# Kernel optimization log

Hardware: AMD Instinct MI355X
Metric: run time of the kernel (lower is better)

## Reference

```python
import jax, jax.numpy as jnp
import numpy as np

EPS = 1e-5

def setup_inputs() -> dict:
    key = jax.random.key(0)
    ks = jax.random.split(key, 8)
    B, C, O, H, W = 4, 256, 256, 64, 64
    x = jax.random.normal(ks[0], (B, C, H, W), jnp.float32)
    # offset/mask conv: 27 = deformable_groups(1) * 3 * kh * kw; small init so sampling points stay near grid
    w_off = jax.random.normal(ks[1], (27, C, 3, 3), jnp.float32) * 0.01
    b_off = jnp.zeros((27,), jnp.float32)
    weight = jax.random.normal(ks[2], (O, C, 3, 3), jnp.float32) * (1.0 / np.sqrt(C * 9))
    bias = jnp.zeros((O,), jnp.float32)
    gamma = 1.0 + 0.1 * jax.random.normal(ks[3], (O,), jnp.float32)
    beta = 0.1 * jax.random.normal(ks[4], (O,), jnp.float32)
    run_mean = 0.05 * jax.random.normal(ks[5], (O,), jnp.float32)
    run_var = jax.random.uniform(ks[6], (O,), jnp.float32, 0.5, 1.5)
    return {"x": x, "w_off": w_off, "b_off": b_off, "weight": weight, "bias": bias,
            "gamma": gamma, "beta": beta, "run_mean": run_mean, "run_var": run_var}

def reference(x, w_off, b_off, weight, bias, gamma, beta, run_mean, run_var):
    B, C, H, W = x.shape
    O = weight.shape[0]
    K = 9  # 3x3 kernel taps
    # conv_offset_mask: standard 3x3 conv, pad 1 -> (B, 27, H, W)
    om = jax.lax.conv_general_dilated(
        x, w_off, window_strides=(1, 1), padding=[(1, 1), (1, 1)],
        dimension_numbers=("NCHW", "OIHW", "NCHW")) + b_off[None, :, None, None]
    dy, dx = om[:, :K], om[:, K:2 * K]            # (B,9,H,W) learned offsets
    mask = jax.nn.sigmoid(om[:, 2 * K:])           # (B,9,H,W) modulation
    # base sampling grid for 3x3, stride 1, pad 1, dilation 1
    ky, kx = jnp.meshgrid(jnp.arange(3), jnp.arange(3), indexing="ij")
    ky = ky.reshape(K, 1, 1).astype(x.dtype)
    kx = kx.reshape(K, 1, 1).astype(x.dtype)
    base_y = (jnp.arange(H, dtype=x.dtype) - 1.0)[None, :, None] + ky  # (9,H,1)
    base_x = (jnp.arange(W, dtype=x.dtype) - 1.0)[None, None, :] + kx  # (9,1,W)
    py = dy + base_y  # (B,9,H,W) absolute sample coords
    px = dx + base_x
    y0 = jnp.floor(py); x0 = jnp.floor(px)
    ly = py - y0; lx = px - x0
    y0i = y0.astype(jnp.int32); x0i = x0.astype(jnp.int32)
    xf = x.reshape(B, C, H * W)

    def corner(yi, xi, wgt):
        valid = (yi >= 0) & (yi < H) & (xi >= 0) & (xi < W)  # zero-pad outside
        yc = jnp.clip(yi, 0, H - 1)
        xc = jnp.clip(xi, 0, W - 1)
        idx = (yc * W + xc).reshape(B, 1, -1)                # (B,1,9HW)
        g = jnp.take_along_axis(xf, idx, axis=2)             # (B,C,9HW)
        return g * (wgt * valid.astype(x.dtype)).reshape(B, 1, -1)

    val = (corner(y0i, x0i, (1 - ly) * (1 - lx))
           + corner(y0i, x0i + 1, (1 - ly) * lx)
           + corner(y0i + 1, x0i, ly * (1 - lx))
           + corner(y0i + 1, x0i + 1, ly * lx))
    val = val.reshape(B, C, K, H, W) * mask[:, None]          # modulated im2col
    out = jnp.einsum("bckhw,ock->bohw", val, weight.reshape(O, C, K))
    out = out + bias[None, :, None, None]
    # BN (eval mode, running stats) + ReLU
    inv = jax.lax.rsqrt(run_var + EPS)
    out = gamma[None, :, None, None] * (out - run_mean[None, :, None, None]) * inv[None, :, None, None] + beta[None, :, None, None]
    return jax.nn.relu(out)
```

## Files before the change

kernel.cpp:

```cpp
#include <hip/hip_runtime.h>
#include <math.h>

#define HW_ 4096
#define N_ 16384
#define RS 592

typedef _Float16 f16x4 __attribute__((ext_vector_type(4)));
typedef _Float16 f16x8 __attribute__((ext_vector_type(8)));
typedef float f32x4 __attribute__((ext_vector_type(4)));


static __device__ __forceinline__ unsigned short f2h(float f) {
  _Float16 h = (_Float16)f;
  return __builtin_bit_cast(unsigned short, h);
}
static __device__ __forceinline__ f32x4 madv(f32x4 a, float s, f32x4 c) {
  c.x = fmaf(a.x, s, c.x);
  c.y = fmaf(a.y, s, c.y);
  c.z = fmaf(a.z, s, c.z);
  c.w = fmaf(a.w, s, c.w);
  return c;
}

__global__ __launch_bounds__(256) void setup_kernel(
    const float* __restrict__ x, const float* __restrict__ weight,
    const float* __restrict__ w_off, const float* __restrict__ bias,
    const float* __restrict__ gamma, const float* __restrict__ beta,
    const float* __restrict__ rmean, const float* __restrict__ rvar,
    unsigned short* __restrict__ Wt, unsigned short* __restrict__ Woff,
    float* __restrict__ scale, float* __restrict__ shift, float* __restrict__ xT) {
  int bid = blockIdx.x;
  int tid = threadIdx.x;
  if (bid < 1024) {
    __shared__ float t[64][65];
    int b = bid >> 8, cg = (bid >> 6) & 3, h = bid & 63;
    int wl = tid & 63, c4 = tid >> 6;
#pragma unroll
    for (int j = 0; j < 16; ++j) {
      int cl = j * 4 + c4;
      t[cl][wl] = x[(size_t)(b * 256 + cg * 64 + cl) * HW_ + h * 64 + wl];
    }
    __syncthreads();
    int cl2 = tid & 63, w4g = tid >> 6;
#pragma unroll
    for (int j = 0; j < 16; ++j) {
      int w2 = j * 4 + w4g;
      xT[(size_t)(b * HW_ + h * 64 + w2) * 256 + cg * 64 + cl2] = t[cl2][w2];
    }
    return;
  }
  int o = bid - 1024;
#pragma unroll
  for (int j = 0; j < 9; ++j) {
    int wk = tid + j * 256;
    int cb = wk / 288;
    int rem = wk - cb * 288;
    int k = rem >> 5, cloc = rem & 31;
    int c = cb * 32 + cloc;
    Wt[((cb * 9 + k) * 256 + o) * 32 + cloc] = f2h(weight[(size_t)(o * 256 + c) * 9 + k]);
    if (o < 32) {
      float wv = (o < 27) ? w_off[(size_t)(o * 256 + c) * 9 + k] : 0.f;
      Woff[((cb * 9 + k) * 32 + o) * 32 + cloc] = f2h(wv);
    }
  }
  if (o == 0) {
    float inv = rsqrtf(rvar[tid] + 1e-5f);
    float sc = gamma[tid] * inv;
    scale[tid] = sc;
    shift[tid] = beta[tid] + sc * (bias[tid] - rmean[tid]);
  }
}

__global__ __launch_bounds__(512) void fused_kernel(
    const float* __restrict__ xT, const unsigned short* __restrict__ Wt,
    const unsigned short* __restrict__ Woff, const float* __restrict__ b_off,
    const float* __restrict__ scale, const float* __restrict__ shift,
    float* __restrict__ out) {
  __shared__ __align__(16) char smem[64 * RS];
  float* om_lds = (float*)smem;
  unsigned int* pk_lds = (unsigned int*)(smem + 8192);
  float* w4_lds = (float*)(smem + 10496);

  int bid = blockIdx.x;
  int swz = (bid & 7) * 32 + (bid >> 3);
  int nbase = swz * 64;
  int b = nbase >> 12;
  int h = (nbase >> 6) & 63;

  int tid = threadIdx.x;
  int lane = tid & 63;
  int wv = tid >> 6;
  int m15 = lane & 15, q = lane >> 4;
  int sn = tid >> 3;
  int cs = tid & 7;

  const char* xb = (const char*)xT + (size_t)b * (HW_ * 256 * 4);

  int mf = wv >> 2, nf1 = wv & 3;
  f32x4 aoff = (f32x4){0.f, 0.f, 0.f, 0.f};
  for (int cb = 0; cb < 8; ++cb) {
    {
      const char* xc = xb + (size_t)(cb * 32 + cs * 4) * 4;
      char* ldr = smem + sn * RS + cs * 8;
#pragma unroll
      for (int k = 0; k < 9; ++k) {
        int ky = k / 3, kx = k - 3 * (k / 3);
        int yy = h + ky - 1, xx = sn + kx - 1;
        f32x4 v = (f32x4){0.f, 0.f, 0.f, 0.f};
        if (((unsigned)yy < 64u) && ((unsigned)xx < 64u))
          v = *(const f32x4*)(xc + (size_t)(yy * 64 + xx) * 1024);
        *(f16x4*)(ldr + k * 64) = __builtin_convertvector(v, f16x4);
      }
    }
    __syncthreads();
#pragma unroll
    for (int ks = 0; ks < 9; ++ks) {
      f16x8 a = *(const f16x8*)(Woff + ((cb * 9 + ks) * 32 + mf * 16 + m15) * 32 + q * 8);
      f16x8 bb = *(const f16x8*)(smem + (nf1 * 16 + m15) * RS + ks * 64 + q * 16);
      aoff = __builtin_amdgcn_mfma_f32_16x16x32_f16(a, bb, aoff, 0, 0, 0);
    }
    __syncthreads();
  }
#pragma unroll
  for (int r = 0; r < 4; ++r)
    om_lds[(mf * 16 + q * 4 + r) * 64 + nf1 * 16 + m15] = aoff[r];
  __syncthreads();

  for (int it = tid; it < 576; it += 512) {
    int k = it >> 6, px = it & 63;
    float dy = om_lds[k * 64 + px] + b_off[k];
    float dx = om_lds[(k + 9) * 64 + px] + b_off[k + 9];
    float z = om_lds[(k + 18) * 64 + px] + b_off[k + 18];
    float ms = 1.f / (1.f + expf(-z));
    int ky = k / 3, kx = k - 3 * ky;
    float py = dy + (float)(h - 1 + ky);
    float pxf = dx + (float)(px - 1 + kx);
    float fy0 = floorf(py), fx0 = floorf(pxf);
    float ly = py - fy0, lx = pxf - fx0;
    int iy0 = (int)fy0, ix0 = (int)fx0;
    bool vy0 = (iy0 >= 0) && (iy0 < 64);
    bool vy1 = (iy0 >= -1) && (iy0 < 63);
    bool vx0 = (ix0 >= 0) && (ix0 < 64);
    bool vx1 = (ix0 >= -1) && (ix0 < 63);
    int yA = min(max(iy0, 0), 63), yB = min(max(iy0 + 1, 0), 63);
    int xA = min(max(ix0, 0), 63), xB = min(max(ix0 + 1, 0), 63);
    pk_lds[k * 64 + px] = (unsigned)(yA * 64 + xA) | ((unsigned)(xB - xA) << 12) |
                          ((unsigned)(yB - yA) << 13);
    float* wp = w4_lds + (k * 64 + px) * 4;
    wp[0] = (1.f - ly) * (1.f - lx) * ms * ((vy0 && vx0) ? 1.f : 0.f);
    wp[1] = (1.f - ly) * lx * ms * ((vy0 && vx1) ? 1.f : 0.f);
    wp[2] = ly * (1.f - lx) * ms * ((vy1 && vx0) ? 1.f : 0.f);
    wp[3] = ly * lx * ms * ((vy1 && vx1) ? 1.f : 0.f);
  }
  __syncthreads();

  unsigned int pkv[9];
  float wf[9][4];
#pragma unroll
  for (int k = 0; k < 9; ++k) {
    pkv[k] = pk_lds[k * 64 + sn];
#pragma unroll
    for (int j = 0; j < 4; ++j) wf[k][j] = w4_lds[(k * 64 + sn) * 4 + j];
  }

  f32x4 acc[2][4];
#pragma unroll
  for (int mfi = 0; mfi < 2; ++mfi)
#pragma unroll
    for (int nf = 0; nf < 4; ++nf) acc[mfi][nf] = (f32x4){0.f, 0.f, 0.f, 0.f};

  f16x4 sv[9];
#define GATHER(CB)                                                     \
  {                                                                    \
    const char* xc = xb + (CB) * 128 + cs * 16;                        \
    _Pragma("unroll") for (int k = 0; k < 9; ++k) {                    \
      unsigned pv = pkv[k];                                            \
      const char* p00 = xc + ((size_t)(pv & 0xFFFu) << 10);            \
      int dxb = (int)(pv & 0x1000u) >> 2;             \
      int dyb = (int)(pv & 0x2000u) << 3;             \
      f32x4 c00 = *(const f32x4*)(p00);                                \
      f32x4 c01 = *(const f32x4*)(p00 + dxb);                          \
      f32x4 c10 = *(const f32x4*)(p00 + dyb);                          \
      f32x4 c11 = *(const f32x4*)(p00 + dyb + dxb);                    \
      f32x4 v = (f32x4){0.f, 0.f, 0.f, 0.f};                           \
      v = madv(c00, wf[k][0], v);                                      \
      v = madv(c01, wf[k][1], v);                                      \
      v = madv(c10, wf[k][2], v);                                      \
      v = madv(c11, wf[k][3], v);                                      \
      sv[k] = __builtin_convertvector(v, f16x4);                       \
    }                                                                  \
  }

  GATHER(0);
  __syncthreads();
  for (int cb = 0; cb < 8; ++cb) {
    {
      char* ldr = smem + sn * RS + cs * 8;
#pragma unroll
      for (int k = 0; k < 9; ++k) *(f16x4*)(ldr + k * 64) = sv[k];
    }
    __syncthreads();
    if (cb < 7) GATHER(cb + 1);
    {
      const unsigned short* wtk = Wt + (size_t)(cb * 9) * 8192 + (wv * 32 + m15) * 32 + q * 8;
#pragma unroll
      for (int ks = 0; ks < 9; ++ks) {
        const unsigned short* wp2 = wtk + ks * 8192;
        f16x8 a0 = *(const f16x8*)(wp2);
        f16x8 a1 = *(const f16x8*)(wp2 + 512);
#pragma unroll
        for (int nf = 0; nf < 4; ++nf) {
          f16x8 bb = *(const f16x8*)(smem + (nf * 16 + m15) * RS + ks * 64 + q * 16);
          acc[0][nf] = __builtin_amdgcn_mfma_f32_16x16x32_f16(a0, bb, acc[0][nf], 0, 0, 0);
          acc[1][nf] = __builtin_amdgcn_mfma_f32_16x16x32_f16(a1, bb, acc[1][nf], 0, 0, 0);
        }
      }
    }
    __syncthreads();
  }

  float* ob = out + (size_t)(b * 256) * HW_ + h * 64;
#pragma unroll
  for (int mfi = 0; mfi < 2; ++mfi)
#pragma unroll
    for (int r = 0; r < 4; ++r) {
      int o = wv * 32 + mfi * 16 + q * 4 + r;
      float sc = scale[o], sh = shift[o];
#pragma unroll
      for (int nf = 0; nf < 4; ++nf) {
        float vv = fmaxf(fmaf(acc[mfi][nf][r], sc, sh), 0.f);
        ob[(size_t)o * HW_ + nf * 16 + m15] = vv;
      }
    }
}

extern "C" void kernel_launch(void* const* d_in, const int* in_sizes, int n_in,
                              void* d_out, int out_size, void* d_ws, size_t ws_size,
                              hipStream_t stream) {
  (void)in_sizes; (void)n_in; (void)out_size; (void)ws_size;
  const float* x = (const float*)d_in[0];
  const float* w_off = (const float*)d_in[1];
  const float* b_off = (const float*)d_in[2];
  const float* weight = (const float*)d_in[3];
  const float* bias = (const float*)d_in[4];
  const float* gamma = (const float*)d_in[5];
  const float* beta = (const float*)d_in[6];
  const float* rmean = (const float*)d_in[7];
  const float* rvar = (const float*)d_in[8];
  char* ws = (char*)d_ws;
  unsigned short* Wt = (unsigned short*)ws;
  unsigned short* Woff = (unsigned short*)(ws + 1179648);
  float* scale = (float*)(ws + 1327104);
  float* shift = (float*)(ws + 1328128);
  float* xT = (float*)(ws + 1329152);
  float* out = (float*)d_out;

  setup_kernel<<<dim3(1280), dim3(256), 0, stream>>>(x, weight, w_off, bias, gamma, beta,
                                                     rmean, rvar, Wt, Woff, scale, shift, xT);
  fused_kernel<<<dim3(256), dim3(512), 0, stream>>>(xT, Wt, Woff, b_off, scale, shift, out);
}
```

Baseline: 192.2 us.

## Halve pixel tile per block, double channel chunk, vectorize transpose setup

The fused deformable-conv kernel now processes 32 output pixels per block instead of 64. It launches 512 blocks so more of the GPU's compute units are busy, and channels are staged in chunks of 64 with a reordered weight layout (18 k-steps per chunk). The setup transpose now uses float4 loads and stores with fewer, larger blocks. Smaller tiles double the weight reads from global/L2 per output, and the offset conv uses only half the waves.

Result: slower. 245.3 us (+27.6%).

```diff
diff --git a/kernel.cpp b/kernel.cpp
--- a/kernel.cpp
+++ b/kernel.cpp
@@ -3,7 +3,7 @@
 
 #define HW_ 4096
 #define N_ 16384
-#define RS 592
+#define RS2 1168
 
 typedef _Float16 f16x4 __attribute__((ext_vector_type(4)));
 typedef _Float16 f16x8 __attribute__((ext_vector_type(8)));
@@ -22,7 +22,7 @@
   return c;
 }
 
-__global__ __launch_bounds__(256) void setup_kernel(
+__global__ __launch_bounds__(512) void setup_kernel(
     const float* __restrict__ x, const float* __restrict__ weight,
     const float* __restrict__ w_off, const float* __restrict__ bias,
     const float* __restrict__ gamma, const float* __restrict__ beta,
@@ -31,110 +31,125 @@
     float* __restrict__ scale, float* __restrict__ shift, float* __restrict__ xT) {
   int bid = blockIdx.x;
   int tid = threadIdx.x;
-  if (bid < 1024) {
+  if (bid < 256) {
     __shared__ float t[64][65];
-    int b = bid >> 8, cg = (bid >> 6) & 3, h = bid & 63;
-    int wl = tid & 63, c4 = tid >> 6;
-#pragma unroll
-    for (int j = 0; j < 16; ++j) {
-      int cl = j * 4 + c4;
-      t[cl][wl] = x[(size_t)(b * 256 + cg * 64 + cl) * HW_ + h * 64 + wl];
-    }
-    __syncthreads();
-    int cl2 = tid & 63, w4g = tid >> 6;
-#pragma unroll
-    for (int j = 0; j < 16; ++j) {
-      int w2 = j * 4 + w4g;
-      xT[(size_t)(b * HW_ + h * 64 + w2) * 256 + cg * 64 + cl2] = t[cl2][w2];
+    int b = bid >> 6, h = bid & 63;
+    int cq = tid & 15, cr = tid >> 4;
+    for (int cg = 0; cg < 4; ++cg) {
+      if (cg) __syncthreads();
+#pragma unroll
+      for (int hf = 0; hf < 2; ++hf) {
+        int cc = cr + hf * 32;
+        f32x4 v = *(const f32x4*)&x[(size_t)(b * 256 + cg * 64 + cc) * HW_ + h * 64 + cq * 4];
+#pragma unroll
+        for (int i2 = 0; i2 < 4; ++i2) t[cc][cq * 4 + i2] = v[i2];
+      }
+      __syncthreads();
+#pragma unroll
+      for (int hf = 0; hf < 2; ++hf) {
+        int w2 = cr + hf * 32;
+        f32x4 v;
+#pragma unroll
+        for (int i2 = 0; i2 < 4; ++i2) v[i2] = t[cq * 4 + i2][w2];
+        *(f32x4*)&xT[(size_t)(b * HW_ + h * 64 + w2) * 256 + cg * 64 + cq * 4] = v;
+      }
     }
     return;
   }
-  int o = bid - 1024;
-#pragma unroll
-  for (int j = 0; j < 9; ++j) {
-    int wk = tid + j * 256;
-    int cb = wk / 288;
-    int rem = wk - cb * 288;
-    int k = rem >> 5, cloc = rem & 31;
-    int c = cb * 32 + cloc;
-    Wt[((cb * 9 + k) * 256 + o) * 32 + cloc] = f2h(weight[(size_t)(o * 256 + c) * 9 + k]);
-    if (o < 32) {
-      float wv = (o < 27) ? w_off[(size_t)(o * 256 + c) * 9 + k] : 0.f;
-      Woff[((cb * 9 + k) * 32 + o) * 32 + cloc] = f2h(wv);
-    }
-  }
-  if (o == 0) {
-    float inv = rsqrtf(rvar[tid] + 1e-5f);
-    float sc = gamma[tid] * inv;
-    scale[tid] = sc;
-    shift[tid] = beta[tid] + sc * (bias[tid] - rmean[tid]);
-  }
-}
-
-__global__ __launch_bounds__(512) void fused_kernel(
+  int o = bid - 256;
+  if (tid < 256) {
+#pragma unroll
+    for (int j = 0; j < 9; ++j) {
+      int wk = tid + j * 256;
+      int cb = wk / 576;
+      int rem = wk - cb * 576;
+      int ks = rem >> 5, cloc = rem & 31;
+      int c = cb * 64 + (ks & 1) * 32 + cloc;
+      int k = ks >> 1;
+      Wt[((cb * 18 + ks) * 256 + o) * 32 + cloc] = f2h(weight[(size_t)(o * 256 + c) * 9 + k]);
+      if (o < 32) {
+        float wv = (o < 27) ? w_off[(size_t)(o * 256 + c) * 9 + k] : 0.f;
+        Woff[((cb * 18 + ks) * 32 + o) * 32 + cloc] = f2h(wv);
+      }
+    }
+    if (o == 0) {
+      float inv = rsqrtf(rvar[tid] + 1e-5f);
+      float sc = gamma[tid] * inv;
+      scale[tid] = sc;
+      shift[tid] = beta[tid] + sc * (bias[tid] - rmean[tid]);
+    }
+  }
+}
+
+__global__ __launch_bounds__(512, 4) void fused_kernel(
     const float* __restrict__ xT, const unsigned short* __restrict__ Wt,
     const unsigned short* __restrict__ Woff, const float* __restrict__ b_off,
     const float* __restrict__ scale, const float* __restrict__ shift,
     float* __restrict__ out) {
-  __shared__ __align__(16) char smem[64 * RS];
+  __shared__ __align__(16) char smem[32 * RS2];
   float* om_lds = (float*)smem;
-  unsigned int* pk_lds = (unsigned int*)(smem + 8192);
-  float* w4_lds = (float*)(smem + 10496);
+  unsigned int* pk_lds = (unsigned int*)(smem + 4096);
+  float* w4_lds = (float*)(smem + 5248);
 
   int bid = blockIdx.x;
-  int swz = (bid & 7) * 32 + (bid >> 3);
-  int nbase = swz * 64;
+  int swz = (bid & 7) * 64 + (bid >> 3);
+  int nbase = swz * 32;
   int b = nbase >> 12;
   int h = (nbase >> 6) & 63;
+  int wb = nbase & 32;
 
   int tid = threadIdx.x;
   int lane = tid & 63;
   int wv = tid >> 6;
   int m15 = lane & 15, q = lane >> 4;
-  int sn = tid >> 3;
-  int cs = tid & 7;
+  int sn = tid >> 4;
+  int cs = tid & 15;
 
   const char* xb = (const char*)xT + (size_t)b * (HW_ * 256 * 4);
-
-  int mf = wv >> 2, nf1 = wv & 3;
+  char* ldr = smem + sn * RS2 + ((cs >> 3) << 6) + (cs & 7) * 8;
+
+  int mf = (wv >> 1) & 1, nf1 = wv & 1;
   f32x4 aoff = (f32x4){0.f, 0.f, 0.f, 0.f};
-  for (int cb = 0; cb < 8; ++cb) {
+  for (int cb = 0; cb < 4; ++cb) {
     {
-      const char* xc = xb + (size_t)(cb * 32 + cs * 4) * 4;
-      char* ldr = smem + sn * RS + cs * 8;
+      const char* xc = xb + cb * 256 + cs * 16;
 #pragma unroll
       for (int k = 0; k < 9; ++k) {
         int ky = k / 3, kx = k - 3 * (k / 3);
-        int yy = h + ky - 1, xx = sn + kx - 1;
+        int yy = h + ky - 1, xx = wb + sn + kx - 1;
         f32x4 v = (f32x4){0.f, 0.f, 0.f, 0.f};
         if (((unsigned)yy < 64u) && ((unsigned)xx < 64u))
           v = *(const f32x4*)(xc + (size_t)(yy * 64 + xx) * 1024);
-        *(f16x4*)(ldr + k * 64) = __builtin_convertvector(v, f16x4);
-      }
-    }
-    __syncthreads();
-#pragma unroll
-    for (int ks = 0; ks < 9; ++ks) {
-      f16x8 a = *(const f16x8*)(Woff + ((cb * 9 + ks) * 32 + mf * 16 + m15) * 32 + q * 8);
-      f16x8 bb = *(const f16x8*)(smem + (nf1 * 16 + m15) * RS + ks * 64 + q * 16);
-      aoff = __builtin_amdgcn_mfma_f32_16x16x32_f16(a, bb, aoff, 0, 0, 0);
-    }
-    __syncthreads();
-  }
-#pragma unroll
-  for (int r = 0; r < 4; ++r)
-    om_lds[(mf * 16 + q * 4 + r) * 64 + nf1 * 16 + m15] = aoff[r];
+        *(f16x4*)(ldr + k * 128) = __builtin_convertvector(v, f16x4);
+      }
+    }
+    __syncthreads();
+    if (wv < 4) {
+#pragma unroll
+      for (int ks = 0; ks < 18; ++ks) {
+        f16x8 a = *(const f16x8*)(Woff + ((cb * 18 + ks) * 32 + mf * 16 + m15) * 32 + q * 8);
+        f16x8 bb = *(const f16x8*)(smem + (nf1 * 16 + m15) * RS2 + ks * 64 + q * 16);
+        aoff = __builtin_amdgcn_mfma_f32_16x16x32_f16(a, bb, aoff, 0, 0, 0);
+      }
+    }
+    __syncthreads();
+  }
+  if (wv < 4) {
+#pragma unroll
+    for (int r = 0; r < 4; ++r)
+      om_lds[(mf * 16 + q * 4 + r) * 32 + nf1 * 16 + m15] = aoff[r];
+  }
   __syncthreads();
 
-  for (int it = tid; it < 576; it += 512) {
-    int k = it >> 6, px = it & 63;
-    float dy = om_lds[k * 64 + px] + b_off[k];
-    float dx = om_lds[(k + 9) * 64 + px] + b_off[k + 9];
-    float z = om_lds[(k + 18) * 64 + px] + b_off[k + 18];
+  if (tid < 288) {
+    int k = tid >> 5, pxl = tid & 31;
+    float dy = om_lds[k * 32 + pxl] + b_off[k];
+    float dx = om_lds[(k + 9) * 32 + pxl] + b_off[k + 9];
+    float z = om_lds[(k + 18) * 32 + pxl] + b_off[k + 18];
     float ms = 1.f / (1.f + expf(-z));
     int ky = k / 3, kx = k - 3 * ky;
     float py = dy + (float)(h - 1 + ky);
-    float pxf = dx + (float)(px - 1 + kx);
+    float pxf = dx + (float)(wb + pxl - 1 + kx);
     float fy0 = floorf(py), fx0 = floorf(pxf);
     float ly = py - fy0, lx = pxf - fx0;
     int iy0 = (int)fy0, ix0 = (int)fx0;
@@ -144,9 +159,9 @@
     bool vx1 = (ix0 >= -1) && (ix0 < 63);
     int yA = min(max(iy0, 0), 63), yB = min(max(iy0 + 1, 0), 63);
     int xA = min(max(ix0, 0), 63), xB = min(max(ix0 + 1, 0), 63);
-    pk_lds[k * 64 + px] = (unsigned)(yA * 64 + xA) | ((unsigned)(xB - xA) << 12) |
-                          ((unsigned)(yB - yA) << 13);
-    float* wp = w4_lds + (k * 64 + px) * 4;
+    pk_lds[k * 32 + pxl] = (unsigned)(yA * 64 + xA) | ((unsigned)(xB - xA) << 12) |
+                           ((unsigned)(yB - yA) << 13);
+    float* wp = w4_lds + (k * 32 + pxl) * 4;
     wp[0] = (1.f - ly) * (1.f - lx) * ms * ((vy0 && vx0) ? 1.f : 0.f);
     wp[1] = (1.f - ly) * lx * ms * ((vy0 && vx1) ? 1.f : 0.f);
     wp[2] = ly * (1.f - lx) * ms * ((vy1 && vx0) ? 1.f : 0.f);
@@ -158,21 +173,21 @@
   float wf[9][4];
 #pragma unroll
   for (int k = 0; k < 9; ++k) {
-    pkv[k] = pk_lds[k * 64 + sn];
-#pragma unroll
-    for (int j = 0; j < 4; ++j) wf[k][j] = w4_lds[(k * 64 + sn) * 4 + j];
-  }
-
-  f32x4 acc[2][4];
+    pkv[k] = pk_lds[k * 32 + sn];
+#pragma unroll
+    for (int j = 0; j < 4; ++j) wf[k][j] = w4_lds[(k * 32 + sn) * 4 + j];
+  }
+
+  f32x4 acc[2][2];
 #pragma unroll
   for (int mfi = 0; mfi < 2; ++mfi)
 #pragma unroll
-    for (int nf = 0; nf < 4; ++nf) acc[mfi][nf] = (f32x4){0.f, 0.f, 0.f, 0.f};
+    for (int nf = 0; nf < 2; ++nf) acc[mfi][nf] = (f32x4){0.f, 0.f, 0.f, 0.f};
 
   f16x4 sv[9];
 #define GATHER(CB)                                                     \
   {                                                                    \
-    const char* xc = xb + (CB) * 128 + cs * 16;                        \
+    const char* xc = xb + (CB) * 256 + cs * 16;                        \
     _Pragma("unroll") for (int k = 0; k < 9; ++k) {                    \
       unsigned pv = pkv[k];                                            \
       const char* p00 = xc + ((size_t)(pv & 0xFFFu) << 10);            \
@@ -193,24 +208,23 @@
 
   GATHER(0);
   __syncthreads();
-  for (int cb = 0; cb < 8; ++cb) {
+  for (int cb = 0; cb < 4; ++cb) {
     {
-      char* ldr = smem + sn * RS + cs * 8;
-#pragma unroll
-      for (int k = 0; k < 9; ++k) *(f16x4*)(ldr + k * 64) = sv[k];
-    }
-    __syncthreads();
-    if (cb < 7) GATHER(cb + 1);
+#pragma unroll
+      for (int k = 0; k < 9; ++k) *(f16x4*)(ldr + k * 128) = sv[k];
+    }
+    __syncthreads();
+    if (cb < 3) GATHER(cb + 1);
     {
-      const unsigned short* wtk = Wt + (size_t)(cb * 9) * 8192 + (wv * 32 + m15) * 32 + q * 8;
-#pragma unroll
-      for (int ks = 0; ks < 9; ++ks) {
+      const unsigned short* wtk = Wt + (size_t)(cb * 18) * 8192 + (wv * 32 + m15) * 32 + q * 8;
+#pragma unroll
+      for (int ks = 0; ks < 18; ++ks) {
         const unsigned short* wp2 = wtk + ks * 8192;
         f16x8 a0 = *(const f16x8*)(wp2);
         f16x8 a1 = *(const f16x8*)(wp2 + 512);
 #pragma unroll
-        for (int nf = 0; nf < 4; ++nf) {
-          f16x8 bb = *(const f16x8*)(smem + (nf * 16 + m15) * RS + ks * 64 + q * 16);
+        for (int nf = 0; nf < 2; ++nf) {
+          f16x8 bb = *(const f16x8*)(smem + (nf * 16 + m15) * RS2 + ks * 64 + q * 16);
           acc[0][nf] = __builtin_amdgcn_mfma_f32_16x16x32_f16(a0, bb, acc[0][nf], 0, 0, 0);
           acc[1][nf] = __builtin_amdgcn_mfma_f32_16x16x32_f16(a1, bb, acc[1][nf], 0, 0, 0);
         }
@@ -219,7 +233,7 @@
     __syncthreads();
   }
 
-  float* ob = out + (size_t)(b * 256) * HW_ + h * 64;
+  float* ob = out + (size_t)(b * 256) * HW_ + h * 64 + wb;
 #pragma unroll
   for (int mfi = 0; mfi < 2; ++mfi)
 #pragma unroll
@@ -227,7 +241,7 @@
       int o = wv * 32 + mfi * 16 + q * 4 + r;
       float sc = scale[o], sh = shift[o];
 #pragma unroll
-      for (int nf = 0; nf < 4; ++nf) {
+      for (int nf = 0; nf < 2; ++nf) {
         float vv = fmaxf(fmaf(acc[mfi][nf][r], sc, sh), 0.f);
         ob[(size_t)o * HW_ + nf * 16 + m15] = vv;
       }
@@ -255,7 +269,7 @@
   float* xT = (float*)(ws + 1329152);
   float* out = (float*)d_out;
 
-  setup_kernel<<<dim3(1280), dim3(256), 0, stream>>>(x, weight, w_off, bias, gamma, beta,
-                                                     rmean, rvar, Wt, Woff, scale, shift, xT);
-  fused_kernel<<<dim3(256), dim3(512), 0, stream>>>(xT, Wt, Woff, b_off, scale, shift, out);
-}
+  setup_kernel<<<dim3(512), dim3(512), 0, stream>>>(x, weight, w_off, bias, gamma, beta,
+                                                    rmean, rvar, Wt, Woff, scale, shift, xT);
+  fused_kernel<<<dim3(512), dim3(512), 0, stream>>>(xT, Wt, Woff, b_off, scale, shift, out);
+}
```
